# Kernel optimization log

Measured on AMD Instinct MI355X. Metric: run time of the kernel, lower is better.

## Reference

```python
import jax, jax.numpy as jnp
import numpy as np

BATCH, SEQ, H, P, HID, CHUNK = 2, 2048, 32, 64, 2048, 256
NORM_EPS = 1e-5


def setup_inputs() -> dict:
    key = jax.random.key(0)
    ks = jax.random.split(key, 10)
    f = lambda k, sh, sc=1.0: jax.random.normal(k, sh, jnp.float32) * sc
    return {
        "hidden_states_ab": f(ks[0], (BATCH, SEQ, HID), 0.02),
        "hidden_states_g": f(ks[1], (BATCH, SEQ, HID), 0.02),
        "q_states": f(ks[2], (BATCH, SEQ, H, P)),
        "k_states": f(ks[3], (BATCH, SEQ, H, P)),
        "v_states": f(ks[4], (BATCH, SEQ, H, P)),
        "dt_w": f(ks[5], (HID, H), 0.02),
        "dt_b": jnp.zeros((H,), jnp.float32),
        "g_w": f(ks[6], (HID, H), 0.02),
        "g_b": jnp.zeros((H,), jnp.float32),
        "A_log": jnp.log(jnp.arange(1, H + 1, dtype=jnp.float32)),
        "dt_bias": jnp.ones((H,), jnp.float32),
        "norm_weight": jnp.ones((H * P,), jnp.float32),
        "o_w": f(ks[7], (H, P, P), 0.02),
        "o_b": jnp.zeros((H, P), jnp.float32),
    }


def _l2norm(x, eps=1e-12):
    # torch F.normalize(p=2, dim=-1): x / max(||x||, eps)
    n = jnp.sqrt(jnp.sum(x * x, axis=-1, keepdims=True))
    return x / jnp.maximum(n, eps)


def _ssd(x, dt, A, Bm, Cm, chunk):
    # x: (b,s,h,p)  dt: (b,s,h) post-softplus  A: (h,)  Bm/Cm: (b,s,h,n)
    b, s, h, p = x.shape
    n = Bm.shape[-1]
    c = s // chunk
    rs = lambda t: t.reshape(b, c, chunk, *t.shape[2:])
    x, dt, Bm, Cm = rs(x), rs(dt), rs(Bm), rs(Cm)
    a = dt * A                         # (b,c,L,h) log-decay increments
    cum = jnp.cumsum(a, axis=2)        # (b,c,L,h)
    cumT = jnp.swapaxes(cum, 2, 3)     # (b,c,h,L)
    # intra-chunk (quadratic, causal) part
    diff = cumT[..., :, None] - cumT[..., None, :]          # (b,c,h,L,L)
    mask = jnp.tril(jnp.ones((chunk, chunk), bool))
    decay = jnp.exp(jnp.where(mask, diff, -jnp.inf))
    CB = jnp.einsum('bclhn,bcshn->bchls', Cm, Bm)
    scores = CB * decay * jnp.swapaxes(dt, 2, 3)[:, :, :, None, :]
    y = jnp.einsum('bchls,bcshp->bclhp', scores, x)
    # per-chunk states
    decay_last = jnp.exp(cumT[..., -1:] - cumT)             # (b,c,h,L)
    w = jnp.swapaxes(decay_last, 2, 3) * dt                 # (b,c,L,h)
    states = jnp.einsum('bclh,bclhn,bclhp->bchpn', w, Bm, x)
    # inter-chunk recurrence over c chunks
    chunk_decay = jnp.exp(cumT[..., -1])                    # (b,c,h)
    def step(Hs, inp):
        cd, st = inp
        return cd[..., None, None] * Hs + st, Hs
    H_last, H_prev = jax.lax.scan(
        step, jnp.zeros((b, h, p, n), x.dtype),
        (jnp.moveaxis(chunk_decay, 1, 0), jnp.moveaxis(states, 1, 0)))
    H_prev = jnp.moveaxis(H_prev, 0, 1)                     # (b,c,h,p,n)
    y = y + jnp.einsum('bclhn,bclh,bchpn->bclhp', Cm, jnp.exp(cum), H_prev)
    return y.reshape(b, s, h, p), H_last


def reference(hidden_states_ab, hidden_states_g, q_states, k_states, v_states,
              dt_w, dt_b, g_w, g_b, A_log, dt_bias, norm_weight, o_w, o_b):
    b, s, h, p = v_states.shape
    Cm = _l2norm(q_states)
    Bm = _l2norm(k_states)
    # dt_proj bias + mamba dt_bias, then softplus (dt_softplus=True)
    dt = jax.nn.softplus(hidden_states_ab @ dt_w + dt_b + dt_bias)   # (b,s,h)
    A = -jnp.exp(A_log)
    y, ssm_state = _ssd(v_states, dt, A, Bm, Cm, CHUNK)
    # gate: g_proj then repeat_interleave(head_dim) on last dim
    gate = jnp.repeat(hidden_states_g @ g_w + g_b, p, axis=-1)       # (b,s,h*p)
    # RMSNormGated, norm_before_gate=False: normalize(x * silu(z)) * weight
    y = y.reshape(b, s, h * p) * jax.nn.silu(gate)
    y = y * jax.lax.rsqrt(jnp.mean(y * y, axis=-1, keepdims=True) + NORM_EPS)
    y = y * norm_weight
    # GroupLinear o_proj: per-head (p -> p) linear
    out = jnp.einsum('bshp,hpq->bshq', y.reshape(b, s, h, p), o_w) + o_b
    return out.reshape(b, s, h * p)
```

## Files before the change

### kernel.cpp

```cpp
#include <hip/hip_runtime.h>
#include <math.h>

#define BATCH 2
#define SEQ   2048
#define NH    32
#define HID   2048
#define CHUNK 256
#define NCH   8
#define NBCH  (BATCH*NCH*NH)
#define PST   72
#define BK    256
#define APST  264
#define KSPLIT 4
#define KSEG  (HID / KSPLIT)

typedef __attribute__((ext_vector_type(4))) float f32x4;
typedef __attribute__((ext_vector_type(8))) short bf16x8;
typedef unsigned int uint;
typedef unsigned short ushort;

__device__ __forceinline__ float softplusf(float x) {
    return x > 20.f ? x : log1pf(expf(x));
}

__device__ __forceinline__ short f2bf(float f) {
    union { float f; uint u; } v; v.f = f;
    uint r = v.u + 0x7FFF + ((v.u >> 16) & 1);
    return (short)(r >> 16);
}
__device__ __forceinline__ float bf2f(ushort s) {
    union { uint u; float f; } v; v.u = ((uint)s) << 16; return v.f;
}
__device__ __forceinline__ uint packbf2(float lo, float hi) {
    return (uint)(ushort)f2bf(lo) | ((uint)(ushort)f2bf(hi) << 16);
}

struct BF8 { union { bf16x8 v; short s[8]; }; };

__device__ __forceinline__ bf16x8 load_cvt8(const float* p, float scale) {
    float4 a = *(const float4*)p;
    float4 b = *(const float4*)(p + 4);
    BF8 r;
    r.s[0]=f2bf(a.x*scale); r.s[1]=f2bf(a.y*scale); r.s[2]=f2bf(a.z*scale); r.s[3]=f2bf(a.w*scale);
    r.s[4]=f2bf(b.x*scale); r.s[5]=f2bf(b.y*scale); r.s[6]=f2bf(b.z*scale); r.s[7]=f2bf(b.w*scale);
    return r.v;
}

__device__ __forceinline__ bf16x8 cvt8(float4 a, float4 b, float s) {
    BF8 r;
    r.s[0]=f2bf(a.x*s); r.s[1]=f2bf(a.y*s); r.s[2]=f2bf(a.z*s); r.s[3]=f2bf(a.w*s);
    r.s[4]=f2bf(b.x*s); r.s[5]=f2bf(b.y*s); r.s[6]=f2bf(b.z*s); r.s[7]=f2bf(b.w*s);
    return r.v;
}

#define MFMA(a,b,c) __builtin_amdgcn_mfma_f32_16x16x32_bf16((a),(b),(c),0,0,0)

__global__ __launch_bounds__(256) void k_proj(
    const float* __restrict__ hs_ab, const float* __restrict__ hs_g,
    const float* __restrict__ dt_w, const float* __restrict__ g_w,
    const float* __restrict__ o_w,  const float* __restrict__ norm_w,
    float* __restrict__ part, short* __restrict__ nwWT)
{
    __shared__ __align__(16) short As[32 * APST];
    __shared__ __align__(16) short Bs[32 * APST];
    int blk = blockIdx.x;
    int t = threadIdx.x;

    if (blk >= 2 * KSPLIT * 128) {
        int h = blk - 2 * KSPLIT * 128;
        float* tile = (float*)As;
        {
            int p = t >> 2, q0 = (t & 3) * 16;
            const float* wp = o_w + (size_t)h * 4096 + p * 64 + q0;
            #pragma unroll
            for (int i = 0; i < 4; ++i)
                *(float4*)(tile + p * 64 + q0 + i * 4) = *(const float4*)(wp + i * 4);
        }
        __syncthreads();
        int q = t >> 2, p0 = (t & 3) * 16;
        uint us[8];
        #pragma unroll
        for (int j = 0; j < 8; ++j) {
            float lo = tile[(p0 + 2*j    ) * 64 + q] * norm_w[h * 64 + p0 + 2*j];
            float hi = tile[(p0 + 2*j + 1) * 64 + q] * norm_w[h * 64 + p0 + 2*j + 1];
            us[j] = packbf2(lo, hi);
        }
        uint* dst = (uint*)(nwWT + (size_t)h * 4096 + q * 64 + p0);
        *(uint4*)dst       = make_uint4(us[0], us[1], us[2], us[3]);
        *(uint4*)(dst + 4) = make_uint4(us[4], us[5], us[6], us[7]);
        return;
    }

    int ksp = blk >> 8;
    int rem = blk & 255;
    int which = rem >> 7;
    int rt = rem & 127;
    int r0 = rt * 32;
    const float* Am = which ? hs_g : hs_ab;
    const float* W  = which ? g_w  : dt_w;
    int w = t >> 6, lane = t & 63, quad = lane >> 4, l16 = lane & 15;
    int mh = w & 1, nh = w >> 1;

    f32x4 acc = (f32x4){0.f, 0.f, 0.f, 0.f};

    for (int kc = ksp * KSEG; kc < ksp * KSEG + KSEG; kc += BK) {
        __syncthreads();
        {
            int row = t >> 3, k0 = (t & 7) * 32;
            const float* src = Am + (size_t)(r0 + row) * HID + kc + k0;
            uint* dst = (uint*)(As + row * APST + k0);
            #pragma unroll
            for (int i = 0; i < 4; ++i) {
                float4 a = *(const float4*)(src + i * 8);
                float4 b = *(const float4*)(src + i * 8 + 4);
                dst[i*4+0] = packbf2(a.x, a.y); dst[i*4+1] = packbf2(a.z, a.w);
                dst[i*4+2] = packbf2(b.x, b.y); dst[i*4+3] = packbf2(b.z, b.w);
            }
        }
        if (t < 128) {
            int k2 = t * 2;
            const float* w0 = W + (size_t)(kc + k2) * NH;
            const float* w1 = w0 + NH;
            #pragma unroll
            for (int n = 0; n < 32; n += 4) {
                float4 a = *(const float4*)(w0 + n);
                float4 b = *(const float4*)(w1 + n);
                *((uint*)(Bs + (n+0) * APST + k2)) = packbf2(a.x, b.x);
                *((uint*)(Bs + (n+1) * APST + k2)) = packbf2(a.y, b.y);
                *((uint*)(Bs + (n+2) * APST + k2)) = packbf2(a.z, b.z);
                *((uint*)(Bs + (n+3) * APST + k2)) = packbf2(a.w, b.w);
            }
        }
        __syncthreads();
        #pragma unroll
        for (int ks = 0; ks < BK / 32; ++ks) {
            bf16x8 af = *(const bf16x8*)(As + (mh*16 + l16) * APST + ks*32 + quad*8);
            bf16x8 bf = *(const bf16x8*)(Bs + (nh*16 + l16) * APST + ks*32 + quad*8);
            acc = MFMA(af, bf, acc);
        }
    }

    int n = nh * 16 + l16;
    int Rb = r0 + mh * 16 + quad * 4;
    float* pd = part + ((size_t)(which * KSPLIT + ksp) * 4096 + Rb) * 32 + n;
    #pragma unroll
    for (int r = 0; r < 4; ++r)
        pd[r * 32] = acc[r];
}

__global__ __launch_bounds__(256) void k_cumsum(
    const float* __restrict__ part, const float* __restrict__ dt_b,
    const float* __restrict__ dt_bias, const float* __restrict__ A_log,
    float* __restrict__ cumc, float* __restrict__ wvc,
    float* __restrict__ dtc, float* __restrict__ cd)
{
    __shared__ float wsum[4];
    int bch = blockIdx.x;
    int h = bch & 31, c = (bch >> 5) & 7, b = bch >> 8;
    int t = threadIdx.x;
    int w = t >> 6, lane = t & 63;
    int rid = (b * SEQ + c * CHUNK + t) * 32 + h;
    float s = part[rid] + part[131072 + rid] + part[262144 + rid] + part[393216 + rid];
    float dt_l = softplusf(s + dt_b[h] + dt_bias[h]);
    float A = -expf(A_log[h]);
    float v = dt_l * A;
    #pragma unroll
    for (int off = 1; off < 64; off <<= 1) {
        float u = __shfl_up(v, off);
        if (lane >= off) v += u;
    }
    if (lane == 63) wsum[w] = v;
    __syncthreads();
    float pre = 0.f;
    #pragma unroll
    for (int i = 0; i < 3; ++i)
        if (i < w) pre += wsum[i];
    float cum = v + pre;
    float tot = wsum[0] + wsum[1] + wsum[2] + wsum[3];
    size_t o = (size_t)bch * CHUNK + t;
    cumc[o] = cum;
    wvc[o] = expf(tot - cum) * dt_l;
    dtc[o] = dt_l;
    if (t == 255) cd[bch] = expf(tot);
}

__global__ __launch_bounds__(256) void k_states(
    const float* __restrict__ kst, const float* __restrict__ vst,
    const float* __restrict__ wvc, float* __restrict__ sp)
{
    __shared__ __align__(16) float kS[64 * 64];
    __shared__ __align__(16) float xS[64 * 64];
    int blk = blockIdx.x;
    int half = blk & 1, bch = blk >> 1;
    int h = bch & 31, c = (bch >> 5) & 7, b = bch >> 8;
    int t = threadIdx.x;
    size_t rowbase = (size_t)b * SEQ + c * CHUNK + half * 128;
    int pg = (t & 15) * 4, ng = (t >> 4) * 4;
    float acc[4][4];
    #pragma unroll
    for (int i = 0; i < 4; ++i)
        #pragma unroll
        for (int j = 0; j < 4; ++j) acc[i][j] = 0.f;

    for (int tt = 0; tt < 2; ++tt) {
        int r0 = t >> 4;
        int c4 = (t & 15) * 4;
        #pragma unroll
        for (int i = 0; i < 4; ++i) {
            int row = r0 + i * 16;
            size_t grow = (rowbase + tt * 64 + row) * NH + h;
            float wv = wvc[(size_t)bch * CHUNK + half * 128 + tt * 64 + row];
            float4 kv = *(const float4*)(kst + grow * 64 + c4);
            float4 xv = *(const float4*)(vst + grow * 64 + c4);
            float ssq = kv.x*kv.x + kv.y*kv.y + kv.z*kv.z + kv.w*kv.w;
            ssq += __shfl_xor(ssq, 1); ssq += __shfl_xor(ssq, 2);
            ssq += __shfl_xor(ssq, 4); ssq += __shfl_xor(ssq, 8);
            float ib = 1.f / fmaxf(sqrtf(ssq), 1e-12f);
            *(float4*)(kS + row * 64 + c4) =
                make_float4(kv.x * ib, kv.y * ib, kv.z * ib, kv.w * ib);
            *(float4*)(xS + row * 64 + c4) =
                make_float4(xv.x * wv, xv.y * wv, xv.z * wv, xv.w * wv);
        }
        __syncthreads();
        for (int ll = 0; ll < 64; ++ll) {
            float4 x4 = *(const float4*)(xS + ll * 64 + pg);
            float4 k4 = *(const float4*)(kS + ll * 64 + ng);
            acc[0][0] += x4.x * k4.x; acc[0][1] += x4.x * k4.y;
            acc[0][2] += x4.x * k4.z; acc[0][3] += x4.x * k4.w;
            acc[1][0] += x4.y * k4.x; acc[1][1] += x4.y * k4.y;
            acc[1][2] += x4.y * k4.z; acc[1][3] += x4.y * k4.w;
            acc[2][0] += x4.z * k4.x; acc[2][1] += x4.z * k4.y;
            acc[2][2] += x4.z * k4.z; acc[2][3] += x4.z * k4.w;
            acc[3][0] += x4.w * k4.x; acc[3][1] += x4.w * k4.y;
            acc[3][2] += x4.w * k4.z; acc[3][3] += x4.w * k4.w;
        }
        __syncthreads();
    }
    size_t obase = (size_t)blk * 4096;
    #pragma unroll
    for (int i = 0; i < 4; ++i)
        *(float4*)(sp + obase + (pg + i) * 64 + ng) =
            make_float4(acc[i][0], acc[i][1], acc[i][2], acc[i][3]);
}

__global__ __launch_bounds__(256) void k_scan(
    const float* __restrict__ sp, const float* __restrict__ cd,
    float* __restrict__ Hp)
{
    size_t id = (size_t)blockIdx.x * 256 + threadIdx.x;
    size_t bh = id >> 12, pn = id & 4095;
    size_t b = bh >> 5, h = bh & 31;
    float carry = 0.f;
    for (int c = 0; c < NCH; ++c) {
        size_t bch = (b * NCH + c) * NH + h;
        float st = sp[(bch * 2) * 4096 + pn] + sp[(bch * 2 + 1) * 4096 + pn];
        Hp[bch * 4096 + pn] = carry;
        carry = cd[bch] * carry + st;
    }
}

__global__ __launch_bounds__(256, 2) void k_intra(
    const float* __restrict__ qst, const float* __restrict__ kst,
    const float* __restrict__ vst,
    const float* __restrict__ cumc, const float* __restrict__ dtc,
    const float* __restrict__ Hp,
    short* __restrict__ ygb)
{
    __shared__ __align__(16) short B_s[64 * PST];
    __shared__ __align__(16) short XT_s[64 * PST];
    __shared__ __align__(16) short P_s[4 * 32 * PST];
    __shared__ float sCum[256];
    __shared__ float sDt[256];

    int bch = blockIdx.x;
    int h = bch & 31, c = (bch >> 5) & 7, b = bch >> 8;
    int t = threadIdx.x;
    int w = t >> 6, lane = t & 63;
    int quad = lane >> 4, l16 = lane & 15;
    size_t rowbase = (size_t)b * SEQ + c * CHUNK;

    sCum[t] = cumc[(size_t)bch * CHUNK + t];
    sDt[t]  = dtc[(size_t)bch * CHUNK + t];
    __syncthreads();

    bf16x8 cf[2][2][2];
    #pragma unroll
    for (int is = 0; is < 2; ++is) {
        int strip = is ? (7 - w) : w;
        #pragma unroll
        for (int lt = 0; lt < 2; ++lt) {
            int l = strip * 32 + lt * 16 + l16;
            size_t grow = (rowbase + l) * NH + h;
            const float* qp = qst + grow * 64 + quad * 8;
            float4 a  = *(const float4*)qp;
            float4 bq = *(const float4*)(qp + 4);
            float4 c2 = *(const float4*)(qp + 32);
            float4 d  = *(const float4*)(qp + 36);
            float ssq = a.x*a.x + a.y*a.y + a.z*a.z + a.w*a.w
                      + bq.x*bq.x + bq.y*bq.y + bq.z*bq.z + bq.w*bq.w
                      + c2.x*c2.x + c2.y*c2.y + c2.z*c2.z + c2.w*c2.w
                      + d.x*d.x + d.y*d.y + d.z*d.z + d.w*d.w;
            ssq += __shfl_xor(ssq, 16);
            ssq += __shfl_xor(ssq, 32);
            float ic = 1.f / fmaxf(sqrtf(ssq), 1e-12f);
            cf[is][lt][0] = cvt8(a, bq, ic);
            cf[is][lt][1] = cvt8(c2, d, ic);
        }
    }

    f32x4 acc[2][2][4];
    #pragma unroll
    for (int is = 0; is < 2; ++is)
        #pragma unroll
        for (int lt = 0; lt < 2; ++lt)
            #pragma unroll
            for (int pt = 0; pt < 4; ++pt)
                acc[is][lt][pt] = (f32x4){0.f, 0.f, 0.f, 0.f};

    {
        bf16x8 hf[4][2];
        #pragma unroll
        for (int pt = 0; pt < 4; ++pt) {
            const float* hp = Hp + (size_t)bch * 4096 + (pt * 16 + l16) * 64 + quad * 8;
            hf[pt][0] = load_cvt8(hp, 1.f);
            hf[pt][1] = load_cvt8(hp + 32, 1.f);
        }
        #pragma unroll
        for (int is = 0; is < 2; ++is)
            #pragma unroll
            for (int lt = 0; lt < 2; ++lt)
                #pragma unroll
                for (int pt = 0; pt < 4; ++pt) {
                    acc[is][lt][pt] = MFMA(cf[is][lt][0], hf[pt][0], acc[is][lt][pt]);
                    acc[is][lt][pt] = MFMA(cf[is][lt][1], hf[pt][1], acc[is][lt][pt]);
                }
    }
    #pragma unroll
    for (int is = 0; is < 2; ++is) {
        int strip = is ? (7 - w) : w;
        #pragma unroll
        for (int lt = 0; lt < 2; ++lt) {
            float e[4];
            #pragma unroll
            for (int r = 0; r < 4; ++r)
                e[r] = __expf(sCum[strip * 32 + lt * 16 + quad * 4 + r]);
            #pragma unroll
            for (int pt = 0; pt < 4; ++pt)
                #pragma unroll
                for (int r = 0; r < 4; ++r)
                    acc[is][lt][pt][r] *= e[r];
        }
    }

    short* Pw = P_s + w * 32 * PST;

    for (int st = 0; st < 4; ++st) {
        __syncthreads();
        {
            int ss = t >> 2, q4 = (t & 3) * 16;
            size_t grow = (rowbase + st * 64 + ss) * NH + h;
            const float4* kp = (const float4*)(kst + grow * 64 + q4);
            float4 v0 = kp[0], v1 = kp[1], v2 = kp[2], v3 = kp[3];
            float ssq = v0.x*v0.x + v0.y*v0.y + v0.z*v0.z + v0.w*v0.w
                      + v1.x*v1.x + v1.y*v1.y + v1.z*v1.z + v1.w*v1.w
                      + v2.x*v2.x + v2.y*v2.y + v2.z*v2.z + v2.w*v2.w
                      + v3.x*v3.x + v3.y*v3.y + v3.z*v3.z + v3.w*v3.w;
            ssq += __shfl_xor(ssq, 1);
            ssq += __shfl_xor(ssq, 2);
            float ib = 1.f / fmaxf(sqrtf(ssq), 1e-12f);
            uint u[8];
            u[0] = packbf2(v0.x * ib, v0.y * ib); u[1] = packbf2(v0.z * ib, v0.w * ib);
            u[2] = packbf2(v1.x * ib, v1.y * ib); u[3] = packbf2(v1.z * ib, v1.w * ib);
            u[4] = packbf2(v2.x * ib, v2.y * ib); u[5] = packbf2(v2.z * ib, v2.w * ib);
            u[6] = packbf2(v3.x * ib, v3.y * ib); u[7] = packbf2(v3.z * ib, v3.w * ib);
            uint* dst = (uint*)(B_s + ss * PST + q4);
            *(uint4*)dst = make_uint4(u[0], u[1], u[2], u[3]);
            *(uint4*)(dst + 4) = make_uint4(u[4], u[5], u[6], u[7]);
        }
        {
            int ss2 = t & 31, qh = t >> 5;
            int p0 = qh * 8;
            size_t g0 = (rowbase + st * 64 + 2 * ss2) * NH + h;
            size_t g1 = g0 + NH;
            float dt0 = sDt[st * 64 + 2 * ss2];
            float dt1 = sDt[st * 64 + 2 * ss2 + 1];
            float4 a0 = *(const float4*)(vst + g0 * 64 + p0);
            float4 a1 = *(const float4*)(vst + g0 * 64 + p0 + 4);
            float4 b0 = *(const float4*)(vst + g1 * 64 + p0);
            float4 b1 = *(const float4*)(vst + g1 * 64 + p0 + 4);
            float x0[8] = {a0.x, a0.y, a0.z, a0.w, a1.x, a1.y, a1.z, a1.w};
            float x1[8] = {b0.x, b0.y, b0.z, b0.w, b1.x, b1.y, b1.z, b1.w};
            uint* xt = (uint*)XT_s;
            #pragma unroll
            for (int i = 0; i < 8; ++i)
                xt[(p0 + i) * (PST / 2) + ss2] = packbf2(x0[i] * dt0, x1[i] * dt1);
        }
        __syncthreads();

        bf16x8 xf[4][2];
        #pragma unroll
        for (int pt = 0; pt < 4; ++pt) {
            #pragma unroll
            for (int ks = 0; ks < 2; ++ks)
                xf[pt][ks] = *(const bf16x8*)(XT_s + (pt * 16 + l16) * PST + ks * 32 + quad * 8);
        }

        #pragma unroll
        for (int is = 0; is < 2; ++is) {
            int strip = is ? (7 - w) : w;
            int L0 = strip * 32;
            if (L0 + 31 < st * 64) continue;

            #pragma unroll
            for (int lt = 0; lt < 2; ++lt) {
                int Lt = L0 + lt * 16;
                float cl = sCum[Lt + l16];
                int lrow = lt * 16 + l16;
                #pragma unroll
                for (int mt = 0; mt < 4; ++mt) {
                    int S0 = st * 64 + mt * 16;
                    uint* pdst = (uint*)(Pw + lrow * PST + mt * 16 + quad * 4);
                    if (S0 > Lt + 15) {
                        *(uint2*)pdst = make_uint2(0u, 0u);
                        continue;
                    }
                    f32x4 sa = (f32x4){0.f, 0.f, 0.f, 0.f};
                    bf16x8 af0 = *(const bf16x8*)(B_s + (mt * 16 + l16) * PST + quad * 8);
                    bf16x8 af1 = *(const bf16x8*)(B_s + (mt * 16 + l16) * PST + 32 + quad * 8);
                    sa = MFMA(af0, cf[is][lt][0], sa);
                    sa = MFMA(af1, cf[is][lt][1], sa);
                    float vals[4];
                    #pragma unroll
                    for (int r = 0; r < 4; ++r) {
                        int s = S0 + quad * 4 + r;
                        float v = sa[r] * __expf(cl - sCum[s]);
                        vals[r] = (Lt + l16 >= s) ? v : 0.f;
                    }
                    *(uint2*)pdst = make_uint2(packbf2(vals[0], vals[1]),
                                               packbf2(vals[2], vals[3]));
                }
            }
            #pragma unroll
            for (int lt = 0; lt < 2; ++lt) {
                int Lmax = L0 + lt * 16 + 15;
                #pragma unroll
                for (int ks = 0; ks < 2; ++ks) {
                    if (st * 64 + ks * 32 > Lmax) continue;
                    bf16x8 af = *(const bf16x8*)(Pw + (lt * 16 + l16) * PST + ks * 32 + quad * 8);
                    #pragma unroll
                    for (int pt = 0; pt < 4; ++pt)
                        acc[is][lt][pt] = MFMA(af, xf[pt][ks], acc[is][lt][pt]);
                }
            }
        }
    }

    #pragma unroll
    for (int is = 0; is < 2; ++is) {
        int strip = is ? (7 - w) : w;
        #pragma unroll
        for (int lt = 0; lt < 2; ++lt)
            #pragma unroll
            for (int pt = 0; pt < 4; ++pt)
                #pragma unroll
                for (int r = 0; r < 4; ++r) {
                    int l = strip * 32 + lt * 16 + quad * 4 + r;
                    int p = pt * 16 + l16;
                    ygb[((rowbase + l) * NH + h) * 64 + p] = f2bf(acc[is][lt][pt][r]);
                }
    }
}

__global__ __launch_bounds__(256) void k_out(
    const short* __restrict__ ygb, const float* __restrict__ part,
    const float* __restrict__ g_b, const short* __restrict__ nwWT,
    const float* __restrict__ o_b, float* __restrict__ out)
{
    __shared__ __align__(16) short yS[16 * 1024];
    __shared__ float silS[16 * 32];
    __shared__ float scaleS[16];
    int blk = blockIdx.x;
    int half = blk & 1, rt = blk >> 1;
    int r0 = rt * 16;
    int t = threadIdx.x;
    int w = t >> 6, lane = t & 63, quad = lane >> 4, l16 = lane & 15;

    const float* gpart = part + 4 * 131072;
    #pragma unroll
    for (int ii = 0; ii < 2; ++ii) {
        int idx = t + ii * 256;
        int rr = idx >> 5, hh = idx & 31;
        int rid = (r0 + rr) * 32 + hh;
        float g = gpart[rid] + gpart[131072 + rid] + gpart[262144 + rid]
                + gpart[393216 + rid] + g_b[hh];
        silS[idx] = g / (1.f + expf(-g));
    }
    __syncthreads();

    int r = t >> 4, cl = t & 15;
    const char* yrow = (const char*)(ygb + (size_t)(r0 + r) * 2048);
    float ssq = 0.f;
    #pragma unroll
    for (int i = 0; i < 16; ++i) {
        int cb = i * 256 + cl * 16;
        uint4 u = *(const uint4*)(yrow + cb);
        float s = silS[r * 32 + (cb >> 7)];
        float v0 = bf2f((ushort)(u.x & 0xFFFF)) * s, v1 = bf2f((ushort)(u.x >> 16)) * s;
        float v2 = bf2f((ushort)(u.y & 0xFFFF)) * s, v3 = bf2f((ushort)(u.y >> 16)) * s;
        float v4 = bf2f((ushort)(u.z & 0xFFFF)) * s, v5 = bf2f((ushort)(u.z >> 16)) * s;
        float v6 = bf2f((ushort)(u.w & 0xFFFF)) * s, v7 = bf2f((ushort)(u.w >> 16)) * s;
        ssq += v0*v0 + v1*v1 + v2*v2 + v3*v3 + v4*v4 + v5*v5 + v6*v6 + v7*v7;
        if ((cb >> 11) == half) {
            int cbl = cb & 2047;
            *(uint4*)((char*)yS + r * 2048 + (cbl ^ ((r & 7) << 4))) = u;
        }
    }
    ssq += __shfl_xor(ssq, 1); ssq += __shfl_xor(ssq, 2);
    ssq += __shfl_xor(ssq, 4); ssq += __shfl_xor(ssq, 8);
    if (cl == 0) scaleS[r] = rsqrtf(ssq / 2048.f + 1e-5f);
    __syncthreads();

    #pragma unroll
    for (int hh = 0; hh < 4; ++hh) {
        int h = half * 16 + w * 4 + hh;
        int hl = h & 15;
        const short* wb = nwWT + (size_t)h * 4096;
        bf16x8 bfr[4][2];
        #pragma unroll
        for (int nt = 0; nt < 4; ++nt)
            #pragma unroll
            for (int ks = 0; ks < 2; ++ks)
                bfr[nt][ks] = *(const bf16x8*)(wb + (nt * 16 + l16) * 64 + ks * 32 + quad * 8);
        bf16x8 af[2];
        #pragma unroll
        for (int ks = 0; ks < 2; ++ks) {
            int cbl = hl * 128 + ks * 64 + quad * 16;
            af[ks] = *(const bf16x8*)((const char*)yS + l16 * 2048 + (cbl ^ ((l16 & 7) << 4)));
        }
        f32x4 acc[4];
        #pragma unroll
        for (int nt = 0; nt < 4; ++nt) acc[nt] = (f32x4){0.f, 0.f, 0.f, 0.f};
        #pragma unroll
        for (int ks = 0; ks < 2; ++ks)
            #pragma unroll
            for (int nt = 0; nt < 4; ++nt)
                acc[nt] = MFMA(af[ks], bfr[nt][ks], acc[nt]);
        #pragma unroll
        for (int nt = 0; nt < 4; ++nt) {
            float bv = o_b[h * 64 + nt * 16 + l16];
            #pragma unroll
            for (int rr = 0; rr < 4; ++rr) {
                int row = quad * 4 + rr;
                float o = acc[nt][rr] * silS[row * 32 + h] * scaleS[row] + bv;
                out[(size_t)(r0 + row) * 2048 + h * 64 + nt * 16 + l16] = o;
            }
        }
    }
}

extern "C" void kernel_launch(void* const* d_in, const int* in_sizes, int n_in,
                              void* d_out, int out_size, void* d_ws, size_t ws_size,
                              hipStream_t stream) {
    const float* hs_ab   = (const float*)d_in[0];
    const float* hs_g    = (const float*)d_in[1];
    const float* qst     = (const float*)d_in[2];
    const float* kst     = (const float*)d_in[3];
    const float* vst     = (const float*)d_in[4];
    const float* dt_w    = (const float*)d_in[5];
    const float* dt_b    = (const float*)d_in[6];
    const float* g_w     = (const float*)d_in[7];
    const float* g_b     = (const float*)d_in[8];
    const float* A_log   = (const float*)d_in[9];
    const float* dt_bias = (const float*)d_in[10];
    const float* norm_w  = (const float*)d_in[11];
    const float* o_w     = (const float*)d_in[12];
    const float* o_b     = (const float*)d_in[13];
    float* out = (float*)d_out;

    float* ws = (float*)d_ws;
    size_t off = 0;
    float* part   = ws + off; off += (size_t)2 * KSPLIT * 4096 * 32;
    float* cumc   = ws + off; off += (size_t)NBCH * CHUNK;
    float* wvc    = ws + off; off += (size_t)NBCH * CHUNK;
    float* dtc    = ws + off; off += (size_t)NBCH * CHUNK;
    float* cd_ws  = ws + off; off += (size_t)NBCH;
    float* sp     = ws + off; off += (size_t)NBCH * 2 * 4096;
    float* Hp     = ws + off; off += (size_t)NBCH * 4096;
    short* nwWT   = (short*)(ws + off); off += (size_t)NH * 64 * 64 / 2;

    short* ygb = (short*)sp;

    k_proj<<<2 * KSPLIT * (BATCH * SEQ / 32) + NH, 256, 0, stream>>>(
        hs_ab, hs_g, dt_w, g_w, o_w, norm_w, part, nwWT);
    k_cumsum<<<NBCH, 256, 0, stream>>>(part, dt_b, dt_bias, A_log,
                                       cumc, wvc, dtc, cd_ws);
    k_states<<<NBCH * 2, 256, 0, stream>>>(kst, vst, wvc, sp);
    k_scan<<<BATCH * NH * 4096 / 256, 256, 0, stream>>>(sp, cd_ws, Hp);
    k_intra<<<NBCH, 256, 0, stream>>>(qst, kst, vst, cumc, dtc, Hp, ygb);
    k_out<<<2 * (BATCH * SEQ / 16), 256, 0, stream>>>(ygb, part, g_b, nwWT, o_b, out);
}
```

Baseline: 270.8 us.

## Double-buffer K/V tiles in k_intra with register prefetch of next stage

The k_intra loop now prefetches the next 64-row K and V tiles into registers while the current stage computes. B_s and XT_s become double-buffered in LDS, which removes the leading barrier of each stage. The first tile's global loads are issued before the C-fragment and Hp work to hide their latency. In exchange, register pressure (16 extra floats per thread, under launch_bounds 256,2) and LDS use both rise, and the loop is fully unrolled.

```diff
diff --git a/kernel.cpp b/kernel.cpp
--- a/kernel.cpp
+++ b/kernel.cpp
@@ -266,8 +266,8 @@
     const float* __restrict__ Hp,
     short* __restrict__ ygb)
 {
-    __shared__ __align__(16) short B_s[64 * PST];
-    __shared__ __align__(16) short XT_s[64 * PST];
+    __shared__ __align__(16) short B_s[2][64 * PST];
+    __shared__ __align__(16) short XT_s[2][64 * PST];
     __shared__ __align__(16) short P_s[4 * 32 * PST];
     __shared__ float sCum[256];
     __shared__ float sDt[256];
@@ -281,7 +281,21 @@
 
     sCum[t] = cumc[(size_t)bch * CHUNK + t];
     sDt[t]  = dtc[(size_t)bch * CHUNK + t];
-    __syncthreads();
+
+    int ssA = t >> 2, q4A = (t & 3) * 16;
+    int ss2 = t & 31, p0 = (t >> 5) * 8;
+
+    float4 kv[4], xa[2], xb[2];
+    {
+        size_t gK = (rowbase + ssA) * NH + h;
+        const float4* kp = (const float4*)(kst + gK * 64 + q4A);
+        kv[0] = kp[0]; kv[1] = kp[1]; kv[2] = kp[2]; kv[3] = kp[3];
+        size_t g0 = (rowbase + 2 * ss2) * NH + h;
+        const float* vp0 = vst + g0 * 64 + p0;
+        const float* vp1 = vst + (g0 + NH) * 64 + p0;
+        xa[0] = *(const float4*)vp0; xa[1] = *(const float4*)(vp0 + 4);
+        xb[0] = *(const float4*)vp1; xb[1] = *(const float4*)(vp1 + 4);
+    }
 
     bf16x8 cf[2][2][2];
     #pragma unroll
@@ -335,6 +349,7 @@
                     acc[is][lt][pt] = MFMA(cf[is][lt][1], hf[pt][1], acc[is][lt][pt]);
                 }
     }
+    __syncthreads();
     #pragma unroll
     for (int is = 0; is < 2; ++is) {
         int strip = is ? (7 - w) : w;
@@ -354,43 +369,47 @@
 
     short* Pw = P_s + w * 32 * PST;
 
+    #pragma unroll
     for (int st = 0; st < 4; ++st) {
-        __syncthreads();
+        float4 kvN[4], xaN[2], xbN[2];
+        if (st < 3) {
+            size_t gK = (rowbase + (st + 1) * 64 + ssA) * NH + h;
+            const float4* kp = (const float4*)(kst + gK * 64 + q4A);
+            kvN[0] = kp[0]; kvN[1] = kp[1]; kvN[2] = kp[2]; kvN[3] = kp[3];
+            size_t g0 = (rowbase + (st + 1) * 64 + 2 * ss2) * NH + h;
+            const float* vp0 = vst + g0 * 64 + p0;
+            const float* vp1 = vst + (g0 + NH) * 64 + p0;
+            xaN[0] = *(const float4*)vp0; xaN[1] = *(const float4*)(vp0 + 4);
+            xbN[0] = *(const float4*)vp1; xbN[1] = *(const float4*)(vp1 + 4);
+        }
+
+        short* Bb = B_s[st & 1];
+        short* Xb = XT_s[st & 1];
         {
-            int ss = t >> 2, q4 = (t & 3) * 16;
-            size_t grow = (rowbase + st * 64 + ss) * NH + h;
-            const float4* kp = (const float4*)(kst + grow * 64 + q4);
-            float4 v0 = kp[0], v1 = kp[1], v2 = kp[2], v3 = kp[3];
-            float ssq = v0.x*v0.x + v0.y*v0.y + v0.z*v0.z + v0.w*v0.w
-                      + v1.x*v1.x + v1.y*v1.y + v1.z*v1.z + v1.w*v1.w
-                      + v2.x*v2.x + v2.y*v2.y + v2.z*v2.z + v2.w*v2.w
-                      + v3.x*v3.x + v3.y*v3.y + v3.z*v3.z + v3.w*v3.w;
+            float ssq = kv[0].x*kv[0].x + kv[0].y*kv[0].y + kv[0].z*kv[0].z + kv[0].w*kv[0].w
+                      + kv[1].x*kv[1].x + kv[1].y*kv[1].y + kv[1].z*kv[1].z + kv[1].w*kv[1].w
+                      + kv[2].x*kv[2].x + kv[2].y*kv[2].y + kv[2].z*kv[2].z + kv[2].w*kv[2].w
+                      + kv[3].x*kv[3].x + kv[3].y*kv[3].y + kv[3].z*kv[3].z + kv[3].w*kv[3].w;
             ssq += __shfl_xor(ssq, 1);
             ssq += __shfl_xor(ssq, 2);
             float ib = 1.f / fmaxf(sqrtf(ssq), 1e-12f);
             uint u[8];
-            u[0] = packbf2(v0.x * ib, v0.y * ib); u[1] = packbf2(v0.z * ib, v0.w * ib);
-            u[2] = packbf2(v1.x * ib, v1.y * ib); u[3] = packbf2(v1.z * ib, v1.w * ib);
-            u[4] = packbf2(v2.x * ib, v2.y * ib); u[5] = packbf2(v2.z * ib, v2.w * ib);
-            u[6] = packbf2(v3.x * ib, v3.y * ib); u[7] = packbf2(v3.z * ib, v3.w * ib);
-            uint* dst = (uint*)(B_s + ss * PST + q4);
+            u[0] = packbf2(kv[0].x * ib, kv[0].y * ib); u[1] = packbf2(kv[0].z * ib, kv[0].w * ib);
+            u[2] = packbf2(kv[1].x * ib, kv[1].y * ib); u[3] = packbf2(kv[1].z * ib, kv[1].w * ib);
+            u[4] = packbf2(kv[2].x * ib, kv[2].y * ib); u[5] = packbf2(kv[2].z * ib, kv[2].w * ib);
+            u[6] = packbf2(kv[3].x * ib, kv[3].y * ib); u[7] = packbf2(kv[3].z * ib, kv[3].w * ib);
+            uint* dst = (uint*)(Bb + ssA * PST + q4A);
             *(uint4*)dst = make_uint4(u[0], u[1], u[2], u[3]);
             *(uint4*)(dst + 4) = make_uint4(u[4], u[5], u[6], u[7]);
         }
         {
-            int ss2 = t & 31, qh = t >> 5;
-            int p0 = qh * 8;
-            size_t g0 = (rowbase + st * 64 + 2 * ss2) * NH + h;
-            size_t g1 = g0 + NH;
             float dt0 = sDt[st * 64 + 2 * ss2];
             float dt1 = sDt[st * 64 + 2 * ss2 + 1];
-            float4 a0 = *(const float4*)(vst + g0 * 64 + p0);
-            float4 a1 = *(const float4*)(vst + g0 * 64 + p0 + 4);
-            float4 b0 = *(const float4*)(vst + g1 * 64 + p0);
-            float4 b1 = *(const float4*)(vst + g1 * 64 + p0 + 4);
-            float x0[8] = {a0.x, a0.y, a0.z, a0.w, a1.x, a1.y, a1.z, a1.w};
-            float x1[8] = {b0.x, b0.y, b0.z, b0.w, b1.x, b1.y, b1.z, b1.w};
-            uint* xt = (uint*)XT_s;
+            float x0[8] = {xa[0].x, xa[0].y, xa[0].z, xa[0].w,
+                           xa[1].x, xa[1].y, xa[1].z, xa[1].w};
+            float x1[8] = {xb[0].x, xb[0].y, xb[0].z, xb[0].w,
+                           xb[1].x, xb[1].y, xb[1].z, xb[1].w};
+            uint* xt = (uint*)Xb;
             #pragma unroll
             for (int i = 0; i < 8; ++i)
                 xt[(p0 + i) * (PST / 2) + ss2] = packbf2(x0[i] * dt0, x1[i] * dt1);
@@ -402,7 +421,7 @@
         for (int pt = 0; pt < 4; ++pt) {
             #pragma unroll
             for (int ks = 0; ks < 2; ++ks)
-                xf[pt][ks] = *(const bf16x8*)(XT_s + (pt * 16 + l16) * PST + ks * 32 + quad * 8);
+                xf[pt][ks] = *(const bf16x8*)(Xb + (pt * 16 + l16) * PST + ks * 32 + quad * 8);
         }
 
         #pragma unroll
@@ -425,8 +444,8 @@
                         continue;
                     }
                     f32x4 sa = (f32x4){0.f, 0.f, 0.f, 0.f};
-                    bf16x8 af0 = *(const bf16x8*)(B_s + (mt * 16 + l16) * PST + quad * 8);
-                    bf16x8 af1 = *(const bf16x8*)(B_s + (mt * 16 + l16) * PST + 32 + quad * 8);
+                    bf16x8 af0 = *(const bf16x8*)(Bb + (mt * 16 + l16) * PST + quad * 8);
+                    bf16x8 af1 = *(const bf16x8*)(Bb + (mt * 16 + l16) * PST + 32 + quad * 8);
                     sa = MFMA(af0, cf[is][lt][0], sa);
                     sa = MFMA(af1, cf[is][lt][1], sa);
                     float vals[4];
@@ -452,6 +471,12 @@
                         acc[is][lt][pt] = MFMA(af, xf[pt][ks], acc[is][lt][pt]);
                 }
             }
+        }
+
+        if (st < 3) {
+            kv[0] = kvN[0]; kv[1] = kvN[1]; kv[2] = kvN[2]; kv[3] = kvN[3];
+            xa[0] = xaN[0]; xa[1] = xaN[1];
+            xb[0] = xbN[0]; xb[1] = xbN[1];
         }
     }
 
```

Measured after the change: 268.3 us. No clear change (-0.9%).
